# Kernel tuning notes

Measured on AMD Instinct MI355X. Metric: run time of the kernel, lower is better.

Reference implementation:

```python
import jax, jax.numpy as jnp
import numpy as np

OUTERCUTOFF = 3.0  # seqm_parameters['pair_outer_cutoff']
NMOL, MOLSIZE = 2048, 100

def setup_inputs() -> dict:
    key = jax.random.key(0)
    k1, k2 = jax.random.split(key)
    species = jax.random.randint(k1, (NMOL, MOLSIZE), 0, 9)          # 0 = blank (padding) atom
    coordinates = jax.random.normal(k2, (NMOL, MOLSIZE, 3), dtype=jnp.float32)
    tore = 2.0 * jnp.arange(10, dtype=jnp.float32)                    # even core charges -> closed shell check passes
    lcf = jnp.float32(1.8897261)                                      # length conversion factor (Angstrom -> Bohr)
    return {"species": species, "coordinates": coordinates, "tore": tore,
            "length_conversion_factor": lcf}

def reference(species, coordinates, tore, length_conversion_factor):
    # NOTE: neighbor-list construction has data-dependent output sizes, so this
    # reference runs eagerly (not under jit) -- that matches the torch original.
    nmol, molsize = species.shape
    nonblank = species > 0                                            # (nmol, molsize)
    flat_nb = nonblank.reshape(-1)
    atom_index = jnp.arange(nmol * molsize)
    real_atoms = atom_index[flat_nb]                                  # compaction of real atoms
    n_real = real_atoms.shape[0]
    inv_real_atoms = jnp.zeros(nmol * molsize, dtype=atom_index.dtype).at[real_atoms].set(
        jnp.arange(n_real))
    Z = species.reshape(-1)[real_atoms]
    nHeavy = jnp.sum(species > 1, axis=1)
    nHydro = jnp.sum(species == 1, axis=1)
    n_charge = jnp.sum(tore[species], axis=1).reshape(-1).astype(jnp.int32)
    if bool(jnp.any(n_charge % 2 == 1)):
        raise ValueError('Only closed shell systems (even electron count) are supported')
    # diagonal indices of each molecule's (molsize x molsize) block
    t1 = (jnp.arange(molsize) * (molsize + 1)).reshape(1, -1)
    t2 = (jnp.arange(nmol) * molsize ** 2).reshape(-1, 1)
    maskd = (t1 + t2).reshape(-1)[real_atoms]
    atom_molid = jnp.repeat(jnp.arange(nmol), molsize)[flat_nb]
    # pair index grids: pair_first[m,i,j] = m*molsize+i ; pair_second[m,i,j] = m*molsize+j
    pair_first = jnp.broadcast_to(atom_index.reshape(nmol, molsize, 1),
                                  (nmol, molsize, molsize)).reshape(-1)
    pair_second = jnp.broadcast_to(atom_index.reshape(nmol, 1, molsize),
                                   (nmol, molsize, molsize)).reshape(-1)
    nonblank_pairs = (nonblank[:, None, :] & nonblank[:, :, None]).reshape(-1)
    # paircoord_raw[m,i,j] = coord[m,j] - coord[m,i]
    paircoord_raw = (coordinates[:, None, :, :] - coordinates[:, :, None, :]).reshape(-1, 3)
    pairdist_sq = jnp.sum(jnp.square(paircoord_raw), axis=1)
    close_pairs = pairdist_sq < OUTERCUTOFF ** 2
    # strict < excludes self-pairs (i==j) which would divide by zero (see notes)
    pairs = (pair_first < pair_second) & nonblank_pairs & close_pairs
    sel = jnp.nonzero(pairs)[0]                                       # data-dependent compaction
    paircoord = paircoord_raw[sel]
    pairdist = jnp.square(pairdist_sq[sel])                           # faithful to source: square, not sqrt
    rij = pairdist * length_conversion_factor
    idxi = inv_real_atoms[pair_first[sel]]
    idxj = inv_real_atoms[pair_second[sel]]
    ni = Z[idxi]
    nj = Z[idxj]
    xij = paircoord / pairdist[:, None]
    mask = real_atoms[idxi] * molsize + real_atoms[idxj] % molsize    # faithful to source precedence
    pair_molid = atom_molid[idxi]
    return (nmol, molsize, nHeavy, nHydro, Z, maskd, atom_molid, mask,
            pair_molid, ni, nj, idxi, idxj, xij, rij)
```

## Files before the change

### kernel.cpp

```cpp
#include <hip/hip_runtime.h>
#include <hip/hip_bf16.h>

#define NMOL    2048
#define MOLSIZE 100
#define MOL2    (MOLSIZE * MOLSIZE)
#define CUTOFF2 9.0f


__global__ __launch_bounds__(256) void k_count(const int* __restrict__ species,
                                               const float* __restrict__ coords,
                                               float* __restrict__ out,
                                               int* __restrict__ ws) {
    const int m = blockIdx.x;
    const int tid = threadIdx.x;
    const int lane = tid & 63, wv = tid >> 6;

    __shared__ float sc[MOLSIZE * 3];
    __shared__ int   ssp[MOLSIZE];
    __shared__ int   s_nb[4], s_hv[4], s_hy[4], s_pc[4];

    for (int t = tid; t < MOLSIZE * 3; t += 256)
        sc[t] = coords[(size_t)m * (MOLSIZE * 3) + t];
    for (int t = tid; t < MOLSIZE; t += 256)
        ssp[t] = species[m * MOLSIZE + t];
    __syncthreads();

    const int sp = (tid < MOLSIZE) ? ssp[tid] : 0;
    unsigned long long bnb = __ballot(sp > 0);
    unsigned long long bhv = __ballot(sp > 1);
    unsigned long long bhy = __ballot(sp == 1);
    if (lane == 0) { s_nb[wv] = __popcll(bnb); s_hv[wv] = __popcll(bhv); s_hy[wv] = __popcll(bhy); }

    int cnt = 0;
    for (int p = tid; p < MOL2; p += 256) {
        const int i = p / MOLSIZE;
        const int j = p - i * MOLSIZE;
        if (i >= j) continue;
        if (ssp[i] <= 0 || ssp[j] <= 0) continue;
        const float dx = __fsub_rn(sc[j * 3 + 0], sc[i * 3 + 0]);
        const float dy = __fsub_rn(sc[j * 3 + 1], sc[i * 3 + 1]);
        const float dz = __fsub_rn(sc[j * 3 + 2], sc[i * 3 + 2]);
        const float d2 = __fadd_rn(__fadd_rn(__fmul_rn(dx, dx), __fmul_rn(dy, dy)),
                                   __fmul_rn(dz, dz));
        if (d2 < CUTOFF2) ++cnt;
    }
    for (int o = 32; o > 0; o >>= 1) cnt += __shfl_down(cnt, o);
    if (lane == 0) s_pc[wv] = cnt;
    __syncthreads();

    if (tid == 0) {
        ws[m]        = s_nb[0] + s_nb[1] + s_nb[2] + s_nb[3];
        ws[NMOL + m] = s_pc[0] + s_pc[1] + s_pc[2] + s_pc[3];
        out[2 + m]          = (float)(s_hv[0] + s_hv[1] + s_hv[2] + s_hv[3]);
        out[2 + NMOL + m]   = (float)(s_hy[0] + s_hy[1] + s_hy[2] + s_hy[3]);
        if (m == 0) { out[0] = (float)NMOL; out[1] = (float)MOLSIZE; }
    }
}

__global__ __launch_bounds__(256) void k_scan(int* __restrict__ ws) {
    const int tid = threadIdx.x, lane = tid & 63, wv = tid >> 6;
    __shared__ int wsum[4];
    for (int which = 0; which < 2; ++which) {
        const int* src = ws + which * NMOL;
        int*       dst = ws + (2 + which) * NMOL;
        int run = 0;
        for (int base = 0; base < NMOL; base += 256) {
            const int v = src[base + tid];
            int x = v;
            for (int o = 1; o < 64; o <<= 1) { int y = __shfl_up(x, o); if (lane >= o) x += y; }
            if (lane == 63) wsum[wv] = x;
            __syncthreads();
            int add = 0;
            for (int w = 0; w < wv; ++w) add += wsum[w];
            const int tot = wsum[0] + wsum[1] + wsum[2] + wsum[3];
            dst[base + tid] = run + add + (x - v);
            run += tot;
            __syncthreads();
        }
        if (tid == 0) ws[4 * NMOL + which] = run;
    }
}

__global__ __launch_bounds__(256) void k_write(const int* __restrict__ species,
                                               const float* __restrict__ coords,
                                               const float* __restrict__ lcf_p,
                                               float* __restrict__ out,
                                               const int* __restrict__ ws) {
    const int m = blockIdx.x;
    const int tid = threadIdx.x;
    const int lane = tid & 63, wv = tid >> 6;

    __shared__ float sc[MOLSIZE * 3];
    __shared__ int   ssp[MOLSIZE];
    __shared__ int   srank[MOLSIZE];
    __shared__ int   wcnt[4];

    for (int t = tid; t < MOLSIZE * 3; t += 256)
        sc[t] = coords[(size_t)m * (MOLSIZE * 3) + t];
    for (int t = tid; t < MOLSIZE; t += 256)
        ssp[t] = species[m * MOLSIZE + t];
    __syncthreads();

    const int atomBase = ws[2 * NMOL + m];
    const int pairBase = ws[3 * NMOL + m];
    const int nReal    = ws[4 * NMOL];
    const int nPairs   = ws[4 * NMOL + 1];
    const float lcf    = lcf_p[0];

    const size_t off_Z      = 2 + 2 * (size_t)NMOL;
    const size_t off_maskd  = off_Z + (size_t)nReal;
    const size_t off_amolid = off_Z + 2 * (size_t)nReal;
    const size_t off_mask   = off_Z + 3 * (size_t)nReal;
    const size_t off_pmolid = off_mask + 1 * (size_t)nPairs;
    const size_t off_ni     = off_mask + 2 * (size_t)nPairs;
    const size_t off_nj     = off_mask + 3 * (size_t)nPairs;
    const size_t off_idxi   = off_mask + 4 * (size_t)nPairs;
    const size_t off_idxj   = off_mask + 5 * (size_t)nPairs;
    const size_t off_xij    = off_mask + 6 * (size_t)nPairs;
    const size_t off_rij    = off_mask + 9 * (size_t)nPairs;

    const int aflag = (tid < MOLSIZE) && (ssp[tid] > 0);
    {
        unsigned long long b = __ballot(aflag);
        const int lanePre = __popcll(b & ((1ull << lane) - 1ull));
        if (lane == 0) wcnt[wv] = __popcll(b);
        __syncthreads();
        int wbase = 0;
        for (int w = 0; w < wv; ++w) wbase += wcnt[w];
        if (aflag) {
            const int r = wbase + lanePre;
            srank[tid] = r;
            const int a = m * MOLSIZE + tid;
            const size_t g = (size_t)atomBase + r;
            out[off_Z + g]      = (float)ssp[tid];
            out[off_maskd + g]  = (float)(a * MOLSIZE + tid);
            out[off_amolid + g] = (float)m;
        }
        __syncthreads();
    }

    int run = pairBase;
    for (int base = 0; base < MOL2; base += 256) {
        const int p = base + tid;
        const int i = p / MOLSIZE;
        const int j = p - i * MOLSIZE;
        float dx = 0.f, dy = 0.f, dz = 0.f, d2 = 0.f;
        bool flag = false;
        if (p < MOL2 && i < j && ssp[i] > 0 && ssp[j] > 0) {
            dx = __fsub_rn(sc[j * 3 + 0], sc[i * 3 + 0]);
            dy = __fsub_rn(sc[j * 3 + 1], sc[i * 3 + 1]);
            dz = __fsub_rn(sc[j * 3 + 2], sc[i * 3 + 2]);
            d2 = __fadd_rn(__fadd_rn(__fmul_rn(dx, dx), __fmul_rn(dy, dy)),
                           __fmul_rn(dz, dz));
            flag = d2 < CUTOFF2;
        }
        unsigned long long bb = __ballot(flag);
        const int lp = __popcll(bb & ((1ull << lane) - 1ull));
        __syncthreads();
        if (lane == 0) wcnt[wv] = __popcll(bb);
        __syncthreads();
        int wb = 0;
        for (int w = 0; w < wv; ++w) wb += wcnt[w];
        const int tot = wcnt[0] + wcnt[1] + wcnt[2] + wcnt[3];
        if (flag) {
            const int r = run + wb + lp;
            const float pd = __fmul_rn(d2, d2);
            out[off_mask + r]   = (float)((m * MOLSIZE + i) * MOLSIZE + j);
            out[off_pmolid + r] = (float)m;
            out[off_ni + r]     = (float)ssp[i];
            out[off_nj + r]     = (float)ssp[j];
            out[off_idxi + r]   = (float)(atomBase + srank[i]);
            out[off_idxj + r]   = (float)(atomBase + srank[j]);
            out[off_xij + 3 * (size_t)r + 0] = __fdiv_rn(dx, pd);
            out[off_xij + 3 * (size_t)r + 1] = __fdiv_rn(dy, pd);
            out[off_xij + 3 * (size_t)r + 2] = __fdiv_rn(dz, pd);
            out[off_rij + r]    = __fmul_rn(pd, lcf);
        }
        run += tot;
    }
}

extern "C" void kernel_launch(void* const* d_in, const int* in_sizes, int n_in,
                              void* d_out, int out_size, void* d_ws, size_t ws_size,
                              hipStream_t stream) {
    const int*   species = (const int*)d_in[0];
    const float* coords  = (const float*)d_in[1];
    const float* lcf     = (const float*)d_in[3];
    float*       out     = (float*)d_out;
    int*         ws      = (int*)d_ws;

    k_count<<<dim3(NMOL), dim3(256), 0, stream>>>(species, coords, out, ws);
    k_scan <<<dim3(1),    dim3(256), 0, stream>>>(ws);
    k_write<<<dim3(NMOL), dim3(256), 0, stream>>>(species, coords, lcf, out, ws);
}
```

Baseline: 304.1 us.

## Iterate only upper-triangle pairs and replace per-chunk block syncs with ballot-mask scan

Both count and write kernels now enumerate the 4950 upper-triangle pairs, decoded from a linear index with a sqrt-based inverse, instead of all 10000 i,j pairs. This removes the half of the work spent on rejected i>=j pairs. The write kernel also stores per-64-pair ballot masks in shared memory, builds chunk offsets with a single-thread serial scan, then scatters outputs in a second pass. That replaces the two __syncthreads per 256-pair iteration, at the cost of recomputing the distances and running a serial 78-step scan.

```diff
diff --git a/kernel.cpp b/kernel.cpp
--- a/kernel.cpp
+++ b/kernel.cpp
@@ -3,9 +3,25 @@
 
 #define NMOL    2048
 #define MOLSIZE 100
-#define MOL2    (MOLSIZE * MOLSIZE)
+#define TRI     4950
+#define NCH     78
 #define CUTOFF2 9.0f
 
+
+__device__ __forceinline__ int tri_row_start(int i) {
+    return 99 * i - (i * (i - 1)) / 2;
+}
+__device__ __forceinline__ void tri_decode(int p, int& i, int& j) {
+    const int disc = 39601 - 8 * p;
+    const float q = sqrtf((float)disc);
+    int ii = (int)((199.0f - q) * 0.5f);
+    if (ii < 0) ii = 0;
+    if (ii > 98) ii = 98;
+    while (tri_row_start(ii + 1) <= p) ++ii;
+    while (tri_row_start(ii) > p) --ii;
+    i = ii;
+    j = ii + 1 + (p - tri_row_start(ii));
+}
 
 __global__ __launch_bounds__(256) void k_count(const int* __restrict__ species,
                                                const float* __restrict__ coords,
@@ -31,28 +47,32 @@
     unsigned long long bhy = __ballot(sp == 1);
     if (lane == 0) { s_nb[wv] = __popcll(bnb); s_hv[wv] = __popcll(bhv); s_hy[wv] = __popcll(bhy); }
 
-    int cnt = 0;
-    for (int p = tid; p < MOL2; p += 256) {
-        const int i = p / MOLSIZE;
-        const int j = p - i * MOLSIZE;
-        if (i >= j) continue;
-        if (ssp[i] <= 0 || ssp[j] <= 0) continue;
-        const float dx = __fsub_rn(sc[j * 3 + 0], sc[i * 3 + 0]);
-        const float dy = __fsub_rn(sc[j * 3 + 1], sc[i * 3 + 1]);
-        const float dz = __fsub_rn(sc[j * 3 + 2], sc[i * 3 + 2]);
-        const float d2 = __fadd_rn(__fadd_rn(__fmul_rn(dx, dx), __fmul_rn(dy, dy)),
-                                   __fmul_rn(dz, dz));
-        if (d2 < CUTOFF2) ++cnt;
-    }
-    for (int o = 32; o > 0; o >>= 1) cnt += __shfl_down(cnt, o);
-    if (lane == 0) s_pc[wv] = cnt;
+    int wcount = 0;
+    for (int c = wv; c < NCH; c += 4) {
+        const int p = c * 64 + lane;
+        bool flag = false;
+        if (p < TRI) {
+            int i, j;
+            tri_decode(p, i, j);
+            if (ssp[i] > 0 && ssp[j] > 0) {
+                const float dx = __fsub_rn(sc[j * 3 + 0], sc[i * 3 + 0]);
+                const float dy = __fsub_rn(sc[j * 3 + 1], sc[i * 3 + 1]);
+                const float dz = __fsub_rn(sc[j * 3 + 2], sc[i * 3 + 2]);
+                const float d2 = __fadd_rn(__fadd_rn(__fmul_rn(dx, dx), __fmul_rn(dy, dy)),
+                                           __fmul_rn(dz, dz));
+                flag = d2 < CUTOFF2;
+            }
+        }
+        wcount += __popcll(__ballot(flag));
+    }
+    if (lane == 0) s_pc[wv] = wcount;
     __syncthreads();
 
     if (tid == 0) {
         ws[m]        = s_nb[0] + s_nb[1] + s_nb[2] + s_nb[3];
         ws[NMOL + m] = s_pc[0] + s_pc[1] + s_pc[2] + s_pc[3];
-        out[2 + m]          = (float)(s_hv[0] + s_hv[1] + s_hv[2] + s_hv[3]);
-        out[2 + NMOL + m]   = (float)(s_hy[0] + s_hy[1] + s_hy[2] + s_hy[3]);
+        out[2 + m]        = (float)(s_hv[0] + s_hv[1] + s_hv[2] + s_hv[3]);
+        out[2 + NMOL + m] = (float)(s_hy[0] + s_hy[1] + s_hy[2] + s_hy[3]);
         if (m == 0) { out[0] = (float)NMOL; out[1] = (float)MOLSIZE; }
     }
 }
@@ -93,6 +113,8 @@
     __shared__ float sc[MOLSIZE * 3];
     __shared__ int   ssp[MOLSIZE];
     __shared__ int   srank[MOLSIZE];
+    __shared__ unsigned long long chBal[NCH];
+    __shared__ int   chOff[NCH];
     __shared__ int   wcnt[4];
 
     for (int t = tid; t < MOLSIZE * 3; t += 256)
@@ -120,50 +142,60 @@
     const size_t off_rij    = off_mask + 9 * (size_t)nPairs;
 
     const int aflag = (tid < MOLSIZE) && (ssp[tid] > 0);
+    const unsigned long long ab = __ballot(aflag);
+    const int aLanePre = __popcll(ab & ((1ull << lane) - 1ull));
+    if (lane == 0) wcnt[wv] = __popcll(ab);
+
+    for (int c = wv; c < NCH; c += 4) {
+        const int p = c * 64 + lane;
+        bool flag = false;
+        if (p < TRI) {
+            int i, j;
+            tri_decode(p, i, j);
+            if (ssp[i] > 0 && ssp[j] > 0) {
+                const float dx = __fsub_rn(sc[j * 3 + 0], sc[i * 3 + 0]);
+                const float dy = __fsub_rn(sc[j * 3 + 1], sc[i * 3 + 1]);
+                const float dz = __fsub_rn(sc[j * 3 + 2], sc[i * 3 + 2]);
+                const float d2 = __fadd_rn(__fadd_rn(__fmul_rn(dx, dx), __fmul_rn(dy, dy)),
+                                           __fmul_rn(dz, dz));
+                flag = d2 < CUTOFF2;
+            }
+        }
+        const unsigned long long bb = __ballot(flag);
+        if (lane == 0) chBal[c] = bb;
+    }
+    __syncthreads();
+
     {
-        unsigned long long b = __ballot(aflag);
-        const int lanePre = __popcll(b & ((1ull << lane) - 1ull));
-        if (lane == 0) wcnt[wv] = __popcll(b);
-        __syncthreads();
         int wbase = 0;
         for (int w = 0; w < wv; ++w) wbase += wcnt[w];
         if (aflag) {
-            const int r = wbase + lanePre;
+            const int r = wbase + aLanePre;
             srank[tid] = r;
-            const int a = m * MOLSIZE + tid;
             const size_t g = (size_t)atomBase + r;
             out[off_Z + g]      = (float)ssp[tid];
-            out[off_maskd + g]  = (float)(a * MOLSIZE + tid);
+            out[off_maskd + g]  = (float)(m * (MOLSIZE * MOLSIZE) + tid * (MOLSIZE + 1));
             out[off_amolid + g] = (float)m;
         }
-        __syncthreads();
-    }
-
-    int run = pairBase;
-    for (int base = 0; base < MOL2; base += 256) {
-        const int p = base + tid;
-        const int i = p / MOLSIZE;
-        const int j = p - i * MOLSIZE;
-        float dx = 0.f, dy = 0.f, dz = 0.f, d2 = 0.f;
-        bool flag = false;
-        if (p < MOL2 && i < j && ssp[i] > 0 && ssp[j] > 0) {
-            dx = __fsub_rn(sc[j * 3 + 0], sc[i * 3 + 0]);
-            dy = __fsub_rn(sc[j * 3 + 1], sc[i * 3 + 1]);
-            dz = __fsub_rn(sc[j * 3 + 2], sc[i * 3 + 2]);
-            d2 = __fadd_rn(__fadd_rn(__fmul_rn(dx, dx), __fmul_rn(dy, dy)),
-                           __fmul_rn(dz, dz));
-            flag = d2 < CUTOFF2;
-        }
-        unsigned long long bb = __ballot(flag);
-        const int lp = __popcll(bb & ((1ull << lane) - 1ull));
-        __syncthreads();
-        if (lane == 0) wcnt[wv] = __popcll(bb);
-        __syncthreads();
-        int wb = 0;
-        for (int w = 0; w < wv; ++w) wb += wcnt[w];
-        const int tot = wcnt[0] + wcnt[1] + wcnt[2] + wcnt[3];
-        if (flag) {
-            const int r = run + wb + lp;
+        if (tid == 255) {
+            int run = 0;
+            for (int c = 0; c < NCH; ++c) { chOff[c] = run; run += __popcll(chBal[c]); }
+        }
+    }
+    __syncthreads();
+
+    for (int c = wv; c < NCH; c += 4) {
+        const unsigned long long bb = chBal[c];
+        if ((bb >> lane) & 1ull) {
+            const int p = c * 64 + lane;
+            int i, j;
+            tri_decode(p, i, j);
+            const float dx = __fsub_rn(sc[j * 3 + 0], sc[i * 3 + 0]);
+            const float dy = __fsub_rn(sc[j * 3 + 1], sc[i * 3 + 1]);
+            const float dz = __fsub_rn(sc[j * 3 + 2], sc[i * 3 + 2]);
+            const float d2 = __fadd_rn(__fadd_rn(__fmul_rn(dx, dx), __fmul_rn(dy, dy)),
+                                       __fmul_rn(dz, dz));
+            const int r = pairBase + chOff[c] + __popcll(bb & ((1ull << lane) - 1ull));
             const float pd = __fmul_rn(d2, d2);
             out[off_mask + r]   = (float)((m * MOLSIZE + i) * MOLSIZE + j);
             out[off_pmolid + r] = (float)m;
@@ -176,7 +208,6 @@
             out[off_xij + 3 * (size_t)r + 2] = __fdiv_rn(dz, pd);
             out[off_rij + r]    = __fmul_rn(pd, lcf);
         }
-        run += tot;
     }
 }
 
```

Result: no change. 306.4 us (+0.8%).
